# Kernel optimization log

Hardware: AMD Instinct MI355X
Metric: run time of the kernel (lower is better)

## Reference

```python
import jax, jax.numpy as jnp
import numpy as np

N = 100_000
D_FEAT = 64
HALF_DEG = 8              # node v connects to v+-o (mod N), o=1..8 -> degree 16
K = 2 * HALF_DEG + 1      # neighborhood incl. self
KNN = 4                   # DifferentiableEmbeddingUTS(k_neighbors=4)
EPS = 1e-12


def setup_inputs() -> dict:
    key = jax.random.key(0)
    kx, k1, k2 = jax.random.split(key, 3)
    x = jax.random.normal(kx, (N, D_FEAT), dtype=jnp.float32)

    offs = np.arange(1, HALF_DEG + 1)
    src = np.repeat(np.arange(N), HALF_DEG)
    dst = (src + np.tile(offs, N)) % N
    edge_index = jnp.asarray(np.stack([src, dst]).astype(np.int64))  # (2, 800k)

    # padded fixed-size neighborhoods: {v} U {v+-o} -- exactly what the
    # original dict/loop builds (set([v]+nbrs[v])), here uniform size K
    all_offs = np.concatenate([[0], offs, -offs])
    nbr_idx = (np.arange(N)[:, None] + all_offs[None, :]) % N
    nbr_idx = jnp.asarray(nbr_idx.astype(np.int64))                  # (N, K)

    W1 = jax.random.normal(k1, (7, 64), dtype=jnp.float32) * 0.1
    b1 = jnp.zeros((64,), dtype=jnp.float32)
    W2 = jax.random.normal(k2, (64, 1), dtype=jnp.float32) * 0.1
    b2 = jnp.zeros((1,), dtype=jnp.float32)
    return {"x": x, "edge_index": edge_index, "nbr_idx": nbr_idx,
            "W1": W1, "b1": b1, "W2": W2, "b2": b2}


def _uts_stats(H):
    """H: (N, K, d) neighborhood embeddings -> (N, 7) differentiable UTS vector.
    Stats: [mean, std, max, min] of centroid distances, mean/std of pairwise
    distances, mean k-NN distance (k=KNN)."""
    n, k, _ = H.shape
    c = H.mean(axis=1, keepdims=True)                         # centroid
    dc = jnp.sqrt(jnp.sum((H - c) ** 2, axis=-1) + EPS)        # (N, K)
    f_mean, f_std = dc.mean(1), dc.std(1)
    f_max, f_min = dc.max(1), dc.min(1)

    sq = jnp.sum(H * H, axis=-1)                               # (N, K)
    D2 = sq[:, :, None] + sq[:, None, :] - 2.0 * jnp.einsum('nkd,nld->nkl', H, H)
    D = jnp.sqrt(jnp.clip(D2, 0.0) + EPS)                      # (N, K, K)

    n_off = k * (k - 1)                                        # off-diagonal count
    pw_mean = D.sum(axis=(1, 2)) / n_off
    pw_m2 = (D * D).sum(axis=(1, 2)) / n_off
    pw_std = jnp.sqrt(jnp.clip(pw_m2 - pw_mean ** 2, 0.0) + EPS)

    Ds = jnp.sort(D, axis=-1)                                  # col 0 is self (=~0)
    knn_mean = Ds[:, :, 1:KNN + 1].mean(axis=(1, 2))

    return jnp.stack([f_mean, f_std, f_max, f_min, pw_mean, pw_std, knn_mean], axis=-1)


def reference(x, edge_index, nbr_idx, W1, b1, W2, b2):
    # edge_index is subsumed by the precomputed padded nbr_idx (same graph).
    H = x[nbr_idx]                     # (N, K, d) ragged gather, padded uniform
    uts = _uts_stats(H)                # (N, 7)
    h = jax.nn.relu(uts @ W1 + b1)     # (N, 64)
    scores = (h @ W2 + b2)[:, 0]       # (N,)
    return scores
```

## Files before the change

kernel.cpp:

```cpp
#include <hip/hip_runtime.h>
#include <math.h>

#define NN     100000
#define K      17
#define HALF   8
#define VB     32
#define NT     128
#define GRID   3125
#define NROWS  48
#define GS     17
#define GRSZ   (NROWS * GS)
#define BS     20
#define FTSZ   (NROWS * BS)
#define EPSF   1e-12f
#define BIGF   3e38f

typedef _Float16 half8v __attribute__((ext_vector_type(8)));
typedef float    f32x4  __attribute__((ext_vector_type(4)));


__global__ __launch_bounds__(NT, 8) void uts_score_kernel(
    const float* __restrict__ x,
    const float* __restrict__ W1,
    const float* __restrict__ b1,
    const float* __restrict__ W2,
    const float* __restrict__ b2,
    float* __restrict__ out)
{
    __shared__ __align__(16) unsigned char smem[7680 + 3264 + 192];
    _Float16* hrows = reinterpret_cast<_Float16*>(smem);
    float2*   ftab  = reinterpret_cast<float2*>(smem);
    float*    graw  = reinterpret_cast<float*>(smem + 7680);
    float*    sqs   = reinterpret_cast<float*>(smem + 7680 + 3264);

    const int tid = threadIdx.x;
    const int v0  = blockIdx.x * VB;

    #pragma unroll
    for (int k = 0; k < 3; ++k) {
        const int idx = tid + NT * k;
        const int r = idx >> 3;
        const int s = idx & 7;
        int gr = v0 - HALF + r;
        if (gr < 0)   gr += NN;
        if (gr >= NN) gr -= NN;
        const float* src = x + (size_t)gr * 64 + s * 8;
        const float4 f0 = *reinterpret_cast<const float4*>(src);
        const float4 f1 = *reinterpret_cast<const float4*>(src + 4);
        half8v h = {(_Float16)f0.x, (_Float16)f0.y, (_Float16)f0.z, (_Float16)f0.w,
                    (_Float16)f1.x, (_Float16)f1.y, (_Float16)f1.z, (_Float16)f1.w};
        *reinterpret_cast<half8v*>(&hrows[r * 64 + ((s ^ (r & 7)) << 3)]) = h;
    }
    __syncthreads();

    {
        const int wid = tid >> 6;
        const int l   = tid & 63;
        const int lr  = l & 15;
        const int kb  = l >> 4;
        #pragma unroll 1
        for (int tp = wid; tp < 5; tp += 2) {
            const int ti = (tp < 3) ? tp : (tp - 3);
            const int tj = (tp < 3) ? tp : (tp - 2);
            const int ra = ti * 16 + lr;
            const int rb = tj * 16 + lr;
            const half8v a0 = *reinterpret_cast<const half8v*>(
                &hrows[ra * 64 + (((kb    ) ^ (ra & 7)) << 3)]);
            const half8v a1 = *reinterpret_cast<const half8v*>(
                &hrows[ra * 64 + (((kb + 4) ^ (ra & 7)) << 3)]);
            half8v b0, b1;
            if (ti == tj) { b0 = a0; b1 = a1; }
            else {
                b0 = *reinterpret_cast<const half8v*>(
                    &hrows[rb * 64 + (((kb    ) ^ (rb & 7)) << 3)]);
                b1 = *reinterpret_cast<const half8v*>(
                    &hrows[rb * 64 + (((kb + 4) ^ (rb & 7)) << 3)]);
            }
            f32x4 c = {0.f, 0.f, 0.f, 0.f};
            c = __builtin_amdgcn_mfma_f32_16x16x32_f16(a0, b0, c, 0, 0, 0);
            c = __builtin_amdgcn_mfma_f32_16x16x32_f16(a1, b1, c, 0, 0, 0);
            const int bcol = tj * 16 + lr;
            #pragma unroll
            for (int r = 0; r < 4; ++r) {
                const int arow = ti * 16 + kb * 4 + r;
                const int d    = bcol - arow;
                if (d >= 0 && d <= 16) {
                    graw[arow * GS + d] = c[r];
                    if (d == 0) sqs[arow] = c[r];
                }
            }
        }
    }
    __syncthreads();

    #pragma unroll
    for (int k = 0; k < 7; ++k) {
        const int idx = tid + NT * k;
        if (idx < GRSZ) {
            const int b = idx / GS;
            const int d = idx - b * GS;
            if (b + d < NROWS) {
                const float g  = graw[idx];
                const float d2 = (d == 0) ? 0.f
                                          : fmaxf(fmaf(-2.f, g, sqs[b] + sqs[b + d]), 0.f);
                float2 e;
                e.x = g;
                e.y = sqrtf(d2 + EPSF);
                ftab[b * BS + d] = e;
            }
        }
    }
    __syncthreads();

    const int nl = tid >> 2;
    const int t  = tid & 3;
    const int v  = v0 + nl;
    const float2* win2 = ftab + nl * BS;

    float sqv[5];
    float psq = 0.f;
    #pragma unroll
    for (int r = 0; r < 5; ++r) {
        const int i = t + 4 * r;
        if (i < K) { sqv[r] = sqs[nl + i]; psq += sqv[r]; }
        else       { sqv[r] = 0.f; }
    }

    float prs = 0.f, pD = 0.f, pknn = 0.f;
    float rsv[5];

    #pragma unroll
    for (int r = 0; r < 5; ++r) {
        const int i = t + 4 * r;
        rsv[r] = 0.f;
        if (i < K) {
            float2 row[17];
            #pragma unroll
            for (int j = 0; j < K; ++j) {
                const int m = (j < i) ? j : i;
                row[j] = win2[18 * m + i + j];
            }
            float rs = 0.f, rowD = 0.f;
            float k0 = BIGF, k1 = BIGF, k2 = BIGF, k3 = BIGF;
            #pragma unroll
            for (int j = 0; j < K; ++j) {
                rs   += row[j].x;
                rowD += row[j].y;
                const float cand = (j == i) ? BIGF : row[j].y;
                const float M0 = fmaxf(k0, cand); k0 = fminf(k0, cand);
                const float M1 = fmaxf(k1, M0);   k1 = fminf(k1, M0);
                const float M2 = fmaxf(k2, M1);   k2 = fminf(k2, M1);
                k3 = fminf(k3, M2);
            }
            rsv[r] = rs;
            prs  += rs;
            pD   += rowD;
            pknn += (k0 + k1) + (k2 + k3);
        }
    }

    psq  += __shfl_xor(psq,  1); psq  += __shfl_xor(psq,  2);
    prs  += __shfl_xor(prs,  1); prs  += __shfl_xor(prs,  2);
    pD   += __shfl_xor(pD,   1); pD   += __shfl_xor(pD,   2);
    pknn += __shfl_xor(pknn, 1); pknn += __shfl_xor(pknn, 2);
    const float sqsum = psq;

    const float pD2 = fmaf(34.f, sqsum, -2.f * prs) + 2.89e-10f;

    const float csq = prs * (1.f / 289.f);
    float dcv[5];
    float dsum = 0.f, dmax = -BIGF, dmin = BIGF;
    #pragma unroll
    for (int r = 0; r < 5; ++r) {
        const int i = t + 4 * r;
        if (i < K) {
            float val = sqv[r] - 2.f * rsv[r] * (1.f / 17.f) + csq + EPSF;
            val = fmaxf(val, 0.f);
            const float dc = sqrtf(val);
            dcv[r] = dc;
            dsum += dc;
            dmax = fmaxf(dmax, dc);
            dmin = fminf(dmin, dc);
        } else {
            dcv[r] = 0.f;
        }
    }
    dsum += __shfl_xor(dsum, 1); dsum += __shfl_xor(dsum, 2);
    dmax = fmaxf(dmax, __shfl_xor(dmax, 1)); dmax = fmaxf(dmax, __shfl_xor(dmax, 2));
    dmin = fminf(dmin, __shfl_xor(dmin, 1)); dmin = fminf(dmin, __shfl_xor(dmin, 2));

    const float f_mean = dsum * (1.f / 17.f);
    float vsum = 0.f;
    #pragma unroll
    for (int r = 0; r < 5; ++r) {
        const int i = t + 4 * r;
        if (i < K) {
            const float d = dcv[r] - f_mean;
            vsum = fmaf(d, d, vsum);
        }
    }
    vsum += __shfl_xor(vsum, 1); vsum += __shfl_xor(vsum, 2);
    const float f_std = sqrtf(vsum * (1.f / 17.f));

    const float pw_mean = pD * (1.f / 272.f);
    const float pw_m2   = pD2 * (1.f / 272.f);
    const float pw_var  = fmaxf(pw_m2 - pw_mean * pw_mean, 0.f);
    const float pw_std  = sqrtf(pw_var + EPSF);
    const float knn_mean = pknn * (1.f / 68.f);

    float uts[7];
    uts[0] = f_mean;
    uts[1] = f_std;
    uts[2] = dmax;
    uts[3] = dmin;
    uts[4] = pw_mean;
    uts[5] = pw_std;
    uts[6] = knn_mean;

    float h[16];
    {
        const float4* b1v = reinterpret_cast<const float4*>(b1 + t * 16);
        #pragma unroll
        for (int q = 0; q < 4; ++q) {
            const float4 bb = b1v[q];
            h[q * 4 + 0] = bb.x; h[q * 4 + 1] = bb.y;
            h[q * 4 + 2] = bb.z; h[q * 4 + 3] = bb.w;
        }
    }
    #pragma unroll
    for (int f = 0; f < 7; ++f) {
        const float uf = uts[f];
        const float4* wrow = reinterpret_cast<const float4*>(W1 + f * 64 + t * 16);
        #pragma unroll
        for (int q = 0; q < 4; ++q) {
            const float4 w = wrow[q];
            h[q * 4 + 0] = fmaf(uf, w.x, h[q * 4 + 0]);
            h[q * 4 + 1] = fmaf(uf, w.y, h[q * 4 + 1]);
            h[q * 4 + 2] = fmaf(uf, w.z, h[q * 4 + 2]);
            h[q * 4 + 3] = fmaf(uf, w.w, h[q * 4 + 3]);
        }
    }
    float score = 0.f;
    {
        const float4* w2v = reinterpret_cast<const float4*>(W2 + t * 16);
        #pragma unroll
        for (int q = 0; q < 4; ++q) {
            const float4 w = w2v[q];
            score = fmaf(fmaxf(h[q * 4 + 0], 0.f), w.x, score);
            score = fmaf(fmaxf(h[q * 4 + 1], 0.f), w.y, score);
            score = fmaf(fmaxf(h[q * 4 + 2], 0.f), w.z, score);
            score = fmaf(fmaxf(h[q * 4 + 3], 0.f), w.w, score);
        }
    }
    score += __shfl_xor(score, 1);
    score += __shfl_xor(score, 2);

    if (t == 0) out[v] = score + b2[0];
}

extern "C" void kernel_launch(void* const* d_in, const int* in_sizes, int n_in,
                              void* d_out, int out_size, void* d_ws, size_t ws_size,
                              hipStream_t stream) {
    const float* x  = (const float*)d_in[0];
    const float* W1 = (const float*)d_in[3];
    const float* b1 = (const float*)d_in[4];
    const float* W2 = (const float*)d_in[5];
    const float* b2 = (const float*)d_in[6];
    float* out = (float*)d_out;

    hipLaunchKernelGGL(uts_score_kernel, dim3(GRID), dim3(NT), 0, stream,
                       x, W1, b1, W2, b2, out);
}
```

Before: 27.66 us.

## Shrink block to 16 nodes in a single wavefront with three MFMA tiles

Halves the nodes per block from 32 to 16 and uses one 64-thread wavefront. That wavefront computes the 32-row banded Gram matrix directly with three 16x16 MFMA tiles: two diagonal and one off-diagonal. Shared memory shrinks and the grid doubles to raise occupancy and drop the cross-wave tile loop. The cost is higher halo overhead, since 32 rows are loaded per 16 nodes instead of 48 per 32, which means more redundant global reads.

```diff
diff --git a/kernel.cpp b/kernel.cpp
--- a/kernel.cpp
+++ b/kernel.cpp
@@ -4,14 +4,13 @@
 #define NN     100000
 #define K      17
 #define HALF   8
-#define VB     32
-#define NT     128
-#define GRID   3125
-#define NROWS  48
+#define VB     16
+#define NT     64
+#define GRID   6250
+#define NROWS  32
 #define GS     17
 #define GRSZ   (NROWS * GS)
 #define BS     20
-#define FTSZ   (NROWS * BS)
 #define EPSF   1e-12f
 #define BIGF   3e38f
 
@@ -19,7 +18,7 @@
 typedef float    f32x4  __attribute__((ext_vector_type(4)));
 
 
-__global__ __launch_bounds__(NT, 8) void uts_score_kernel(
+__global__ __launch_bounds__(NT, 5) void uts_score_kernel(
     const float* __restrict__ x,
     const float* __restrict__ W1,
     const float* __restrict__ b1,
@@ -27,17 +26,17 @@
     const float* __restrict__ b2,
     float* __restrict__ out)
 {
-    __shared__ __align__(16) unsigned char smem[7680 + 3264 + 192];
+    __shared__ __align__(16) unsigned char smem[5120 + 2176 + 128];
     _Float16* hrows = reinterpret_cast<_Float16*>(smem);
     float2*   ftab  = reinterpret_cast<float2*>(smem);
-    float*    graw  = reinterpret_cast<float*>(smem + 7680);
-    float*    sqs   = reinterpret_cast<float*>(smem + 7680 + 3264);
+    float*    graw  = reinterpret_cast<float*>(smem + 5120);
+    float*    sqs   = reinterpret_cast<float*>(smem + 5120 + 2176);
 
     const int tid = threadIdx.x;
     const int v0  = blockIdx.x * VB;
 
     #pragma unroll
-    for (int k = 0; k < 3; ++k) {
+    for (int k = 0; k < 4; ++k) {
         const int idx = tid + NT * k;
         const int r = idx >> 3;
         const int s = idx & 7;
@@ -54,47 +53,49 @@
     __syncthreads();
 
     {
-        const int wid = tid >> 6;
-        const int l   = tid & 63;
-        const int lr  = l & 15;
-        const int kb  = l >> 4;
-        #pragma unroll 1
-        for (int tp = wid; tp < 5; tp += 2) {
-            const int ti = (tp < 3) ? tp : (tp - 3);
-            const int tj = (tp < 3) ? tp : (tp - 2);
-            const int ra = ti * 16 + lr;
-            const int rb = tj * 16 + lr;
-            const half8v a0 = *reinterpret_cast<const half8v*>(
-                &hrows[ra * 64 + (((kb    ) ^ (ra & 7)) << 3)]);
-            const half8v a1 = *reinterpret_cast<const half8v*>(
-                &hrows[ra * 64 + (((kb + 4) ^ (ra & 7)) << 3)]);
-            half8v b0, b1;
-            if (ti == tj) { b0 = a0; b1 = a1; }
-            else {
-                b0 = *reinterpret_cast<const half8v*>(
-                    &hrows[rb * 64 + (((kb    ) ^ (rb & 7)) << 3)]);
-                b1 = *reinterpret_cast<const half8v*>(
-                    &hrows[rb * 64 + (((kb + 4) ^ (rb & 7)) << 3)]);
-            }
-            f32x4 c = {0.f, 0.f, 0.f, 0.f};
-            c = __builtin_amdgcn_mfma_f32_16x16x32_f16(a0, b0, c, 0, 0, 0);
-            c = __builtin_amdgcn_mfma_f32_16x16x32_f16(a1, b1, c, 0, 0, 0);
-            const int bcol = tj * 16 + lr;
-            #pragma unroll
-            for (int r = 0; r < 4; ++r) {
-                const int arow = ti * 16 + kb * 4 + r;
-                const int d    = bcol - arow;
-                if (d >= 0 && d <= 16) {
-                    graw[arow * GS + d] = c[r];
-                    if (d == 0) sqs[arow] = c[r];
-                }
-            }
+        const int lr = tid & 15;
+        const int kb = tid >> 4;
+        const int r0 = lr;
+        const int r1 = 16 + lr;
+        const half8v a0 = *reinterpret_cast<const half8v*>(
+            &hrows[r0 * 64 + (((kb    ) ^ (r0 & 7)) << 3)]);
+        const half8v a1 = *reinterpret_cast<const half8v*>(
+            &hrows[r0 * 64 + (((kb + 4) ^ (r0 & 7)) << 3)]);
+        const half8v b0 = *reinterpret_cast<const half8v*>(
+            &hrows[r1 * 64 + (((kb    ) ^ (r1 & 7)) << 3)]);
+        const half8v b1 = *reinterpret_cast<const half8v*>(
+            &hrows[r1 * 64 + (((kb + 4) ^ (r1 & 7)) << 3)]);
+
+        f32x4 c00 = {0.f, 0.f, 0.f, 0.f};
+        c00 = __builtin_amdgcn_mfma_f32_16x16x32_f16(a0, a0, c00, 0, 0, 0);
+        c00 = __builtin_amdgcn_mfma_f32_16x16x32_f16(a1, a1, c00, 0, 0, 0);
+        f32x4 c11 = {0.f, 0.f, 0.f, 0.f};
+        c11 = __builtin_amdgcn_mfma_f32_16x16x32_f16(b0, b0, c11, 0, 0, 0);
+        c11 = __builtin_amdgcn_mfma_f32_16x16x32_f16(b1, b1, c11, 0, 0, 0);
+        f32x4 c01 = {0.f, 0.f, 0.f, 0.f};
+        c01 = __builtin_amdgcn_mfma_f32_16x16x32_f16(a0, b0, c01, 0, 0, 0);
+        c01 = __builtin_amdgcn_mfma_f32_16x16x32_f16(a1, b1, c01, 0, 0, 0);
+
+        #pragma unroll
+        for (int r = 0; r < 4; ++r) {
+            const int ar = kb * 4 + r;
+            int d = lr - ar;
+            if (d >= 0) {
+                graw[ar * GS + d] = c00[r];
+                if (d == 0) sqs[ar] = c00[r];
+            }
+            if (d >= 0) {
+                graw[(16 + ar) * GS + d] = c11[r];
+                if (d == 0) sqs[16 + ar] = c11[r];
+            }
+            const int d2 = 16 + lr - ar;
+            if (d2 <= 16) graw[ar * GS + d2] = c01[r];
         }
     }
     __syncthreads();
 
     #pragma unroll
-    for (int k = 0; k < 7; ++k) {
+    for (int k = 0; k < 9; ++k) {
         const int idx = tid + NT * k;
         if (idx < GRSZ) {
             const int b = idx / GS;
```

After: 28.32 us. 2.4% more time.
